# Optimization experiments

Hardware: AMD Instinct MI355X
Metric: run time of the kernel (lower is better)

Reference implementation:

```python
import jax, jax.numpy as jnp
import numpy as np

K_NEIGHBORS = 8  # sparse_reads


def setup_inputs() -> dict:
    key = jax.random.key(0)
    k1, k2, k3, k4 = jax.random.split(key, 4)
    b, m, w, r, d_in = 32, 65536, 32, 4, 256
    xi = jax.random.normal(k1, (b, d_in), jnp.float32)
    sparse = jax.random.normal(k2, (b, m, w), jnp.float32)
    W_rk = jax.random.normal(k3, (r * w, d_in), jnp.float32) * 0.05  # read_keys_transform weight
    b_rk = jax.random.normal(k4, (r * w,), jnp.float32) * 0.01       # read_keys_transform bias
    return {"xi": xi, "sparse": sparse, "W_rk": W_rk, "b_rk": b_rk}


def reference(xi, sparse, W_rk, b_rk):
    b = xi.shape[0]
    m, w = sparse.shape[1], sparse.shape[2]
    r = W_rk.shape[0] // w
    # read keys: Linear(input_size, r*w) -> [b, r, w]
    read_keys = (xi @ W_rk.T + b_rk).reshape(b, r, w)
    # exact kNN replacing FLANN: squared L2 distances [b, r, m]
    d2 = (
        jnp.sum(read_keys * read_keys, -1)[..., None]
        - 2.0 * jnp.einsum('brw,bmw->brm', read_keys, sparse)
        + jnp.sum(sparse * sparse, -1)[:, None, :]
    )
    neg_d, idx = jax.lax.top_k(-d2, K_NEIGHBORS)  # K smallest distances
    dist = -neg_d                                  # [b, r, K]
    # gather the K nearest memory rows per (batch, head): [b, r, K, w]
    vecs = sparse[jnp.arange(b)[:, None, None], idx]
    # distances normalized by their max (per key), as in `distances / max(distances)`
    read_weights = dist / jnp.max(dist, -1, keepdims=True)
    # torch code stacks per-key over batch then over keys -> [r, b, K, w]
    read_vectors = jnp.transpose(vecs, (1, 0, 2, 3))
    read_weights = jnp.transpose(read_weights, (1, 0, 2))  # [r, b, K]
    return read_vectors, read_weights
```

## Files before the change

### kernel.cpp

```cpp
#include <hip/hip_runtime.h>

constexpr int Bb = 32;
constexpr int Mm = 65536;
constexpr int Ww = 32;
constexpr int Rr = 4;
constexpr int Dd = 256;
constexpr int Kk = 8;

constexpr int NB_A = 64;
constexpr int TPB_A = 256;
constexpr int ROWS_PER_BLOCK = Mm / NB_A;
constexpr int TILE_ROWS = 128;
constexpr int TILES = ROWS_PER_BLOCK / TILE_ROWS;
constexpr int NBUF = 3;
constexpr int CPL = NB_A * Kk / 64;

__device__ __forceinline__ void glds16(const float4* src, float4* dst_lds) {
  __builtin_amdgcn_global_load_lds(
      (const __attribute__((address_space(1))) void*)src,
      (__attribute__((address_space(3))) void*)dst_lds, 16, 0, 0);
}

__global__ __launch_bounds__(128) void rk_kernel(
    const float* __restrict__ xi, const float* __restrict__ Wrk,
    const float* __restrict__ brk, float* __restrict__ rk,
    float* __restrict__ rknorm) {
  const int b = blockIdx.x;
  const int tid = threadIdx.x;
  __shared__ float xs[Dd];
  __shared__ float rks[Rr * Ww];
  #pragma unroll
  for (int i = 0; i < Dd; i += 128) xs[i + tid] = xi[b * Dd + i + tid];
  __syncthreads();
  float acc = brk[tid];
  const float4* wr = reinterpret_cast<const float4*>(Wrk + (size_t)tid * Dd);
  #pragma unroll 4
  for (int i = 0; i < Dd / 4; ++i) {
    float4 wv = wr[i];
    acc = fmaf(wv.x, xs[4 * i + 0], acc);
    acc = fmaf(wv.y, xs[4 * i + 1], acc);
    acc = fmaf(wv.z, xs[4 * i + 2], acc);
    acc = fmaf(wv.w, xs[4 * i + 3], acc);
  }
  rk[b * Rr * Ww + tid] = acc;
  rks[tid] = acc;
  __syncthreads();
  if (tid < Rr) {
    float s = 0.f;
    #pragma unroll
    for (int j = 0; j < Ww; ++j) s = fmaf(rks[tid * Ww + j], rks[tid * Ww + j], s);
    rknorm[b * Rr + tid] = s;
  }
}

__global__ __launch_bounds__(TPB_A, 2) void topk_partial(
    const float* __restrict__ sparse, const float* __restrict__ rk,
    const float* __restrict__ rknorm, float* __restrict__ cand_d,
    int* __restrict__ cand_i) {
  const int b = blockIdx.y;
  const int tid = threadIdx.x;
  const int lane = tid & 63;
  const int wid = tid >> 6;
  const float INF = __builtin_inff();

  __shared__ float4 rk4[Rr][8];
  __shared__ float rkn_s[Rr];
  __shared__ float4 tile[NBUF][TILE_ROWS * 8];

  if (tid < Rr * Ww) reinterpret_cast<float*>(rk4)[tid] = rk[b * Rr * Ww + tid];
  if (tid < Rr) rkn_s[tid] = rknorm[b * Rr + tid];
  __syncthreads();

  float rkn[Rr];
  #pragma unroll
  for (int r = 0; r < Rr; ++r) rkn[r] = rkn_s[r];

  const int rowBlk = blockIdx.x * ROWS_PER_BLOCK;
  const float4* sb4 =
      reinterpret_cast<const float4*>(sparse) + (size_t)b * Mm * 8;
  const int perm = ((lane >> 3) * 8) + ((lane & 7) ^ (lane >> 3));

  const int rowL = wid * 32 + (lane >> 1);
  const int rmask = rowL & 7;
  const int hsel = (tid & 1) * 4;

  float d8[Rr][TILES];

  auto STAGE = [&](int buf, int t) {
    const float4* g0 = sb4 + (size_t)(rowBlk + t * TILE_ROWS + wid * 32) * 8;
    float4* l0 = &tile[buf][wid * 32 * 8];
    #pragma unroll
    for (int i = 0; i < 4; ++i) glds16(g0 + i * 64 + perm, l0 + i * 64);
  };

  STAGE(0, 0);
  STAGE(1, 1);
  #pragma unroll
  for (int t = 0; t < TILES; ++t) {
    if (t + 2 < TILES) {
      asm volatile("s_waitcnt lgkmcnt(0)" ::: "memory");
      STAGE((t + 2) % NBUF, t + 2);
      asm volatile("s_waitcnt vmcnt(8)" ::: "memory");
    } else if (t + 1 < TILES) {
      asm volatile("s_waitcnt vmcnt(4)" ::: "memory");
    } else {
      asm volatile("s_waitcnt vmcnt(0)" ::: "memory");
    }
    const float4* tb = &tile[t % NBUF][rowL * 8];
    float a0 = 0.f, a1 = 0.f, a2 = 0.f, a3 = 0.f, ss = 0.f;
    #pragma unroll
    for (int j = 0; j < 4; ++j) {
      float4 v = tb[(hsel + j) ^ rmask];
      float4 k0 = rk4[0][hsel + j];
      float4 k1 = rk4[1][hsel + j];
      float4 k2 = rk4[2][hsel + j];
      float4 k3 = rk4[3][hsel + j];
      a0 = fmaf(k0.x, v.x, a0); a0 = fmaf(k0.y, v.y, a0);
      a0 = fmaf(k0.z, v.z, a0); a0 = fmaf(k0.w, v.w, a0);
      a1 = fmaf(k1.x, v.x, a1); a1 = fmaf(k1.y, v.y, a1);
      a1 = fmaf(k1.z, v.z, a1); a1 = fmaf(k1.w, v.w, a1);
      a2 = fmaf(k2.x, v.x, a2); a2 = fmaf(k2.y, v.y, a2);
      a2 = fmaf(k2.z, v.z, a2); a2 = fmaf(k2.w, v.w, a2);
      a3 = fmaf(k3.x, v.x, a3); a3 = fmaf(k3.y, v.y, a3);
      a3 = fmaf(k3.z, v.z, a3); a3 = fmaf(k3.w, v.w, a3);
      ss = fmaf(v.x, v.x, ss); ss = fmaf(v.y, v.y, ss);
      ss = fmaf(v.z, v.z, ss); ss = fmaf(v.w, v.w, ss);
    }
    float p0 = fmaf(-2.f, a0, ss);
    float p1 = fmaf(-2.f, a1, ss);
    float p2 = fmaf(-2.f, a2, ss);
    float p3 = fmaf(-2.f, a3, ss);
    p0 += __shfl_xor(p0, 1);
    p1 += __shfl_xor(p1, 1);
    p2 += __shfl_xor(p2, 1);
    p3 += __shfl_xor(p3, 1);
    d8[0][t] = p0 + rkn[0];
    d8[1][t] = p1 + rkn[1];
    d8[2][t] = p2 + rkn[2];
    d8[3][t] = p3 + rkn[3];
  }

  __syncthreads();
  float* dmp = reinterpret_cast<float*>(&tile[0][0]);
  if ((tid & 1) == 0) {
    const int e = tid >> 1;
    #pragma unroll
    for (int r = 0; r < Rr; ++r) {
      float4* p = reinterpret_cast<float4*>(&dmp[(r * 128 + e) * 8]);
      p[0] = make_float4(d8[r][0], d8[r][1], d8[r][2], d8[r][3]);
      p[1] = make_float4(d8[r][4], d8[r][5], d8[r][6], d8[r][7]);
    }
  }
  __syncthreads();

  {
    const int r = wid;
    const int e0 = 2 * lane;
    float v[2][8];
    #pragma unroll
    for (int q = 0; q < 2; ++q) {
      const float4* p =
          reinterpret_cast<const float4*>(&dmp[(r * 128 + e0 + q) * 8]);
      float4 lo = p[0], hi = p[1];
      v[q][0] = lo.x; v[q][1] = lo.y; v[q][2] = lo.z; v[q][3] = lo.w;
      v[q][4] = hi.x; v[q][5] = hi.y; v[q][6] = hi.z; v[q][7] = hi.w;
    }
    const int base = rowBlk + e0;
    size_t o = ((size_t)(b * Rr + r) * NB_A + blockIdx.x) * Kk;
    #pragma unroll
    for (int k = 0; k < Kk; ++k) {
      float lv = v[0][0];
      int lrow = base;
      #pragma unroll
      for (int q = 0; q < 2; ++q)
        #pragma unroll
        for (int s = 0; s < 8; ++s) {
          if (q == 0 && s == 0) continue;
          int row = base + q + s * TILE_ROWS;
          if (v[q][s] < lv || (v[q][s] == lv && row < lrow)) {
            lv = v[q][s]; lrow = row;
          }
        }
      float bv = lv;
      int bi = lrow;
      #pragma unroll
      for (int off = 32; off; off >>= 1) {
        float ov = __shfl_xor(bv, off);
        int oi = __shfl_xor(bi, off);
        if (ov < bv || (ov == bv && oi < bi)) { bv = ov; bi = oi; }
      }
      if (lane == 0) { cand_d[o + k] = bv; cand_i[o + k] = bi; }
      #pragma unroll
      for (int q = 0; q < 2; ++q)
        #pragma unroll
        for (int s = 0; s < 8; ++s) {
          bool clr = (v[q][s] == bv) && (base + q + s * TILE_ROWS == bi);
          v[q][s] = clr ? INF : v[q][s];
        }
    }
  }
}

__global__ __launch_bounds__(64) void topk_final(
    const float* __restrict__ sparse, const float* __restrict__ cand_d,
    const int* __restrict__ cand_i, float* __restrict__ out) {
  const int br = blockIdx.x;
  const int b = br >> 2;
  const int r = br & 3;
  const int lane = threadIdx.x;
  const float INF = __builtin_inff();

  float ld[CPL];
  int li[CPL];
  const float* cd = cand_d + (size_t)br * (NB_A * Kk);
  const int* ci = cand_i + (size_t)br * (NB_A * Kk);
  #pragma unroll
  for (int t = 0; t < CPL; ++t) {
    ld[t] = cd[t * 64 + lane];
    li[t] = ci[t * 64 + lane];
  }
  #pragma unroll
  for (int i = 0; i < CPL - 1; ++i)
    #pragma unroll
    for (int j = 0; j < CPL - 1 - i; ++j)
      if (ld[j + 1] < ld[j] || (ld[j + 1] == ld[j] && li[j + 1] < li[j])) {
        float td = ld[j]; ld[j] = ld[j + 1]; ld[j + 1] = td;
        int ti = li[j]; li[j] = li[j + 1]; li[j + 1] = ti;
      }

  __shared__ float s_td[Kk];
  __shared__ int s_ti[Kk];
  #pragma unroll
  for (int k = 0; k < Kk; ++k) {
    float v = ld[0];
    int id = li[0];
    #pragma unroll
    for (int off = 32; off; off >>= 1) {
      float ov = __shfl_xor(v, off);
      int oi = __shfl_xor(id, off);
      if (ov < v || (ov == v && oi < id)) { v = ov; id = oi; }
    }
    if (lane == 0) { s_td[k] = v; s_ti[k] = id; }
    if (li[0] == id) {
      #pragma unroll
      for (int j = 0; j < CPL - 1; ++j) { ld[j] = ld[j + 1]; li[j] = li[j + 1]; }
      ld[CPL - 1] = INF;
      li[CPL - 1] = -1;
    }
  }
  __syncthreads();

  const float dmax = s_td[Kk - 1];
  if (lane < Kk)
    out[(size_t)Rr * Bb * Kk * Ww + ((size_t)r * Bb + b) * Kk + lane] =
        s_td[lane] / dmax;

  const float* sbase = sparse + (size_t)b * Mm * Ww;
  #pragma unroll
  for (int t = 0; t < (Kk * Ww) / 64; ++t) {
    int e = t * 64 + lane;
    int k = e >> 5;
    int j = e & 31;
    out[(((size_t)r * Bb + b) * Kk + k) * Ww + j] =
        sbase[(size_t)s_ti[k] * Ww + j];
  }
}

extern "C" void kernel_launch(void* const* d_in, const int* in_sizes, int n_in,
                              void* d_out, int out_size, void* d_ws,
                              size_t ws_size, hipStream_t stream) {
  const float* xi = (const float*)d_in[0];
  const float* sparse = (const float*)d_in[1];
  const float* Wrk = (const float*)d_in[2];
  const float* brk = (const float*)d_in[3];
  float* out = (float*)d_out;

  char* ws = (char*)d_ws;
  float* rk = (float*)ws;
  float* rknorm = (float*)(ws + 16384);
  float* cand_d = (float*)(ws + 16896);
  int* cand_i = (int*)(ws + 16896 + 262144);

  rk_kernel<<<Bb, 128, 0, stream>>>(xi, Wrk, brk, rk, rknorm);
  dim3 gridA(NB_A, Bb);
  topk_partial<<<gridA, TPB_A, 0, stream>>>(sparse, rk, rknorm, cand_d, cand_i);
  topk_final<<<Bb * Rr, 64, 0, stream>>>(sparse, cand_d, cand_i, out);
}
```

Baseline: 92.04 us.

## Double partial-topk blocks, cache read keys in registers, defer norm add

```diff
diff --git a/kernel.cpp b/kernel.cpp
--- a/kernel.cpp
+++ b/kernel.cpp
@@ -7,7 +7,7 @@
 constexpr int Dd = 256;
 constexpr int Kk = 8;
 
-constexpr int NB_A = 64;
+constexpr int NB_A = 128;
 constexpr int TPB_A = 256;
 constexpr int ROWS_PER_BLOCK = Mm / NB_A;
 constexpr int TILE_ROWS = 128;
@@ -71,10 +71,6 @@
   if (tid < Rr) rkn_s[tid] = rknorm[b * Rr + tid];
   __syncthreads();
 
-  float rkn[Rr];
-  #pragma unroll
-  for (int r = 0; r < Rr; ++r) rkn[r] = rkn_s[r];
-
   const int rowBlk = blockIdx.x * ROWS_PER_BLOCK;
   const float4* sb4 =
       reinterpret_cast<const float4*>(sparse) + (size_t)b * Mm * 8;
@@ -83,6 +79,12 @@
   const int rowL = wid * 32 + (lane >> 1);
   const int rmask = rowL & 7;
   const int hsel = (tid & 1) * 4;
+
+  float4 rkq[Rr][4];
+  #pragma unroll
+  for (int r = 0; r < Rr; ++r)
+    #pragma unroll
+    for (int j = 0; j < 4; ++j) rkq[r][j] = rk4[r][hsel + j];
 
   float d8[Rr][TILES];
 
@@ -111,10 +113,10 @@
     #pragma unroll
     for (int j = 0; j < 4; ++j) {
       float4 v = tb[(hsel + j) ^ rmask];
-      float4 k0 = rk4[0][hsel + j];
-      float4 k1 = rk4[1][hsel + j];
-      float4 k2 = rk4[2][hsel + j];
-      float4 k3 = rk4[3][hsel + j];
+      float4 k0 = rkq[0][j];
+      float4 k1 = rkq[1][j];
+      float4 k2 = rkq[2][j];
+      float4 k3 = rkq[3][j];
       a0 = fmaf(k0.x, v.x, a0); a0 = fmaf(k0.y, v.y, a0);
       a0 = fmaf(k0.z, v.z, a0); a0 = fmaf(k0.w, v.w, a0);
       a1 = fmaf(k1.x, v.x, a1); a1 = fmaf(k1.y, v.y, a1);
@@ -134,10 +136,10 @@
     p1 += __shfl_xor(p1, 1);
     p2 += __shfl_xor(p2, 1);
     p3 += __shfl_xor(p3, 1);
-    d8[0][t] = p0 + rkn[0];
-    d8[1][t] = p1 + rkn[1];
-    d8[2][t] = p2 + rkn[2];
-    d8[3][t] = p3 + rkn[3];
+    d8[0][t] = p0;
+    d8[1][t] = p1;
+    d8[2][t] = p2;
+    d8[3][t] = p3;
   }
 
   __syncthreads();
@@ -146,9 +148,8 @@
     const int e = tid >> 1;
     #pragma unroll
     for (int r = 0; r < Rr; ++r) {
-      float4* p = reinterpret_cast<float4*>(&dmp[(r * 128 + e) * 8]);
-      p[0] = make_float4(d8[r][0], d8[r][1], d8[r][2], d8[r][3]);
-      p[1] = make_float4(d8[r][4], d8[r][5], d8[r][6], d8[r][7]);
+      *reinterpret_cast<float4*>(&dmp[(r * 128 + e) * 4]) =
+          make_float4(d8[r][0], d8[r][1], d8[r][2], d8[r][3]);
     }
   }
   __syncthreads();
@@ -156,14 +157,12 @@
   {
     const int r = wid;
     const int e0 = 2 * lane;
-    float v[2][8];
+    const float rknr = rkn_s[r];
+    float v[2][TILES];
     #pragma unroll
     for (int q = 0; q < 2; ++q) {
-      const float4* p =
-          reinterpret_cast<const float4*>(&dmp[(r * 128 + e0 + q) * 8]);
-      float4 lo = p[0], hi = p[1];
+      float4 lo = *reinterpret_cast<const float4*>(&dmp[(r * 128 + e0 + q) * 4]);
       v[q][0] = lo.x; v[q][1] = lo.y; v[q][2] = lo.z; v[q][3] = lo.w;
-      v[q][4] = hi.x; v[q][5] = hi.y; v[q][6] = hi.z; v[q][7] = hi.w;
     }
     const int base = rowBlk + e0;
     size_t o = ((size_t)(b * Rr + r) * NB_A + blockIdx.x) * Kk;
@@ -174,7 +173,7 @@
       #pragma unroll
       for (int q = 0; q < 2; ++q)
         #pragma unroll
-        for (int s = 0; s < 8; ++s) {
+        for (int s = 0; s < TILES; ++s) {
           if (q == 0 && s == 0) continue;
           int row = base + q + s * TILE_ROWS;
           if (v[q][s] < lv || (v[q][s] == lv && row < lrow)) {
@@ -189,11 +188,11 @@
         int oi = __shfl_xor(bi, off);
         if (ov < bv || (ov == bv && oi < bi)) { bv = ov; bi = oi; }
       }
-      if (lane == 0) { cand_d[o + k] = bv; cand_i[o + k] = bi; }
+      if (lane == 0) { cand_d[o + k] = bv + rknr; cand_i[o + k] = bi; }
       #pragma unroll
       for (int q = 0; q < 2; ++q)
         #pragma unroll
-        for (int s = 0; s < 8; ++s) {
+        for (int s = 0; s < TILES; ++s) {
           bool clr = (v[q][s] == bv) && (base + q + s * TILE_ROWS == bi);
           v[q][s] = clr ? INF : v[q][s];
         }
@@ -243,7 +242,11 @@
     if (lane == 0) { s_td[k] = v; s_ti[k] = id; }
     if (li[0] == id) {
       #pragma unroll
-      for (int j = 0; j < CPL - 1; ++j) { ld[j] = ld[j + 1]; li[j] = li[j + 1]; }
+      for (int j = 0; j < Kk - 1; ++j) { ld[j] = ld[j + 1]; li[j] = li[j + 1]; }
+      ld[Kk - 1] = ld[Kk];
+      li[Kk - 1] = li[Kk];
+      #pragma unroll
+      for (int j = Kk; j < CPL - 1; ++j) { ld[j] = ld[j + 1]; li[j] = li[j + 1]; }
       ld[CPL - 1] = INF;
       li[CPL - 1] = -1;
     }
@@ -279,7 +282,7 @@
   float* rk = (float*)ws;
   float* rknorm = (float*)(ws + 16384);
   float* cand_d = (float*)(ws + 16896);
-  int* cand_i = (int*)(ws + 16896 + 262144);
+  int* cand_i = (int*)(ws + 16896 + 524288);
 
   rk_kernel<<<Bb, 128, 0, stream>>>(xi, Wrk, brk, rk, rknorm);
   dim3 gridA(NB_A, Bb);
```

Result: slower. 130.7 us (+42.0%).

## Split heads across lane pairs and keep read keys in registers

Applied to the files above, without the earlier changes.

```diff
diff --git a/kernel.cpp b/kernel.cpp
--- a/kernel.cpp
+++ b/kernel.cpp
@@ -71,20 +71,28 @@
   if (tid < Rr) rkn_s[tid] = rknorm[b * Rr + tid];
   __syncthreads();
 
-  float rkn[Rr];
-  #pragma unroll
-  for (int r = 0; r < Rr; ++r) rkn[r] = rkn_s[r];
-
   const int rowBlk = blockIdx.x * ROWS_PER_BLOCK;
   const float4* sb4 =
       reinterpret_cast<const float4*>(sparse) + (size_t)b * Mm * 8;
   const int perm = ((lane >> 3) * 8) + ((lane & 7) ^ (lane >> 3));
 
-  const int rowL = wid * 32 + (lane >> 1);
-  const int rmask = rowL & 7;
-  const int hsel = (tid & 1) * 4;
-
-  float d8[Rr][TILES];
+  const int pr = lane >> 2;
+  const int sub = lane & 3;
+  const int hg = sub >> 1;
+  const int ch = sub & 1;
+  const int rowL0 = wid * 32 + pr;
+  const int h0 = hg * 2, h1 = h0 + 1;
+
+  float4 ka[4], kb[4];
+  #pragma unroll
+  for (int j = 0; j < 4; ++j) {
+    ka[j] = rk4[h0][ch * 4 + j];
+    kb[j] = rk4[h1][ch * 4 + j];
+  }
+  const float rknA = rkn_s[h0];
+  const float rknB = rkn_s[h1];
+
+  float d8[2][2 * TILES];
 
   auto STAGE = [&](int buf, int t) {
     const float4* g0 = sb4 + (size_t)(rowBlk + t * TILE_ROWS + wid * 32) * 8;
@@ -106,65 +114,54 @@
     } else {
       asm volatile("s_waitcnt vmcnt(0)" ::: "memory");
     }
-    const float4* tb = &tile[t % NBUF][rowL * 8];
-    float a0 = 0.f, a1 = 0.f, a2 = 0.f, a3 = 0.f, ss = 0.f;
-    #pragma unroll
-    for (int j = 0; j < 4; ++j) {
-      float4 v = tb[(hsel + j) ^ rmask];
-      float4 k0 = rk4[0][hsel + j];
-      float4 k1 = rk4[1][hsel + j];
-      float4 k2 = rk4[2][hsel + j];
-      float4 k3 = rk4[3][hsel + j];
-      a0 = fmaf(k0.x, v.x, a0); a0 = fmaf(k0.y, v.y, a0);
-      a0 = fmaf(k0.z, v.z, a0); a0 = fmaf(k0.w, v.w, a0);
-      a1 = fmaf(k1.x, v.x, a1); a1 = fmaf(k1.y, v.y, a1);
-      a1 = fmaf(k1.z, v.z, a1); a1 = fmaf(k1.w, v.w, a1);
-      a2 = fmaf(k2.x, v.x, a2); a2 = fmaf(k2.y, v.y, a2);
-      a2 = fmaf(k2.z, v.z, a2); a2 = fmaf(k2.w, v.w, a2);
-      a3 = fmaf(k3.x, v.x, a3); a3 = fmaf(k3.y, v.y, a3);
-      a3 = fmaf(k3.z, v.z, a3); a3 = fmaf(k3.w, v.w, a3);
-      ss = fmaf(v.x, v.x, ss); ss = fmaf(v.y, v.y, ss);
-      ss = fmaf(v.z, v.z, ss); ss = fmaf(v.w, v.w, ss);
-    }
-    float p0 = fmaf(-2.f, a0, ss);
-    float p1 = fmaf(-2.f, a1, ss);
-    float p2 = fmaf(-2.f, a2, ss);
-    float p3 = fmaf(-2.f, a3, ss);
-    p0 += __shfl_xor(p0, 1);
-    p1 += __shfl_xor(p1, 1);
-    p2 += __shfl_xor(p2, 1);
-    p3 += __shfl_xor(p3, 1);
-    d8[0][t] = p0 + rkn[0];
-    d8[1][t] = p1 + rkn[1];
-    d8[2][t] = p2 + rkn[2];
-    d8[3][t] = p3 + rkn[3];
+    #pragma unroll
+    for (int q = 0; q < 2; ++q) {
+      const int row = rowL0 + q * 16;
+      const int rmask = row & 7;
+      const float4* tb = &tile[t % NBUF][row * 8];
+      float a0 = 0.f, a1 = 0.f, ss = 0.f;
+      #pragma unroll
+      for (int j = 0; j < 4; ++j) {
+        float4 v = tb[(ch * 4 + j) ^ rmask];
+        a0 = fmaf(ka[j].x, v.x, a0); a0 = fmaf(ka[j].y, v.y, a0);
+        a0 = fmaf(ka[j].z, v.z, a0); a0 = fmaf(ka[j].w, v.w, a0);
+        a1 = fmaf(kb[j].x, v.x, a1); a1 = fmaf(kb[j].y, v.y, a1);
+        a1 = fmaf(kb[j].z, v.z, a1); a1 = fmaf(kb[j].w, v.w, a1);
+        ss = fmaf(v.x, v.x, ss); ss = fmaf(v.y, v.y, ss);
+        ss = fmaf(v.z, v.z, ss); ss = fmaf(v.w, v.w, ss);
+      }
+      float pA = fmaf(-2.f, a0, ss);
+      float pB = fmaf(-2.f, a1, ss);
+      pA += __shfl_xor(pA, 1);
+      pB += __shfl_xor(pB, 1);
+      d8[0][t * 2 + q] = pA + rknA;
+      d8[1][t * 2 + q] = pB + rknB;
+    }
   }
 
   __syncthreads();
   float* dmp = reinterpret_cast<float*>(&tile[0][0]);
-  if ((tid & 1) == 0) {
-    const int e = tid >> 1;
-    #pragma unroll
-    for (int r = 0; r < Rr; ++r) {
-      float4* p = reinterpret_cast<float4*>(&dmp[(r * 128 + e) * 8]);
-      p[0] = make_float4(d8[r][0], d8[r][1], d8[r][2], d8[r][3]);
-      p[1] = make_float4(d8[r][4], d8[r][5], d8[r][6], d8[r][7]);
-    }
+  if (ch == 0) {
+    #pragma unroll
+    for (int t = 0; t < TILES; ++t)
+      #pragma unroll
+      for (int q = 0; q < 2; ++q) {
+        const int rit = rowL0 + q * 16;
+        dmp[h0 * ROWS_PER_BLOCK + t * TILE_ROWS + rit] = d8[0][t * 2 + q];
+        dmp[h1 * ROWS_PER_BLOCK + t * TILE_ROWS + rit] = d8[1][t * 2 + q];
+      }
   }
   __syncthreads();
 
   {
     const int r = wid;
     const int e0 = 2 * lane;
-    float v[2][8];
-    #pragma unroll
-    for (int q = 0; q < 2; ++q) {
-      const float4* p =
-          reinterpret_cast<const float4*>(&dmp[(r * 128 + e0 + q) * 8]);
-      float4 lo = p[0], hi = p[1];
-      v[q][0] = lo.x; v[q][1] = lo.y; v[q][2] = lo.z; v[q][3] = lo.w;
-      v[q][4] = hi.x; v[q][5] = hi.y; v[q][6] = hi.z; v[q][7] = hi.w;
-    }
+    float v[2][TILES];
+    #pragma unroll
+    for (int q = 0; q < 2; ++q)
+      #pragma unroll
+      for (int s = 0; s < TILES; ++s)
+        v[q][s] = dmp[r * ROWS_PER_BLOCK + s * TILE_ROWS + e0 + q];
     const int base = rowBlk + e0;
     size_t o = ((size_t)(b * Rr + r) * NB_A + blockIdx.x) * Kk;
     #pragma unroll
@@ -174,7 +171,7 @@
       #pragma unroll
       for (int q = 0; q < 2; ++q)
         #pragma unroll
-        for (int s = 0; s < 8; ++s) {
+        for (int s = 0; s < TILES; ++s) {
           if (q == 0 && s == 0) continue;
           int row = base + q + s * TILE_ROWS;
           if (v[q][s] < lv || (v[q][s] == lv && row < lrow)) {
@@ -193,7 +190,7 @@
       #pragma unroll
       for (int q = 0; q < 2; ++q)
         #pragma unroll
-        for (int s = 0; s < 8; ++s) {
+        for (int s = 0; s < TILES; ++s) {
           bool clr = (v[q][s] == bv) && (base + q + s * TILE_ROWS == bi);
           v[q][s] = clr ? INF : v[q][s];
         }
```

Result: no change. 90.28 us (-1.9%).
